# Performance work log

Measured on AMD Instinct MI355X. Metric: run time of the kernel, lower is better.

The kernel has to match this reference:

```python
import jax, jax.numpy as jnp
import numpy as np

B, T, C, H, L, V = 2, 2048, 1024, 16, 6, 32000
D = C // H
FF = 4 * C
EPS = 1e-5


def setup_inputs() -> dict:
    key = jax.random.key(0)
    ks = iter(jax.random.split(key, 32))
    s = 0.02
    inp = {
        "src": jax.random.randint(next(ks), (B, T), 0, V),
        "src_emb": jax.random.normal(next(ks), (V, C), jnp.float32) * s,
        "pos_emb": jax.random.normal(next(ks), (T, C), jnp.float32) * s,
        # stacked per-layer params, leading dim L
        "ln1_w": jnp.ones((L, C), jnp.float32),
        "ln1_b": jnp.zeros((L, C), jnp.float32),
        "wq": jax.random.normal(next(ks), (L, C, C), jnp.float32) * s,
        "bq": jnp.zeros((L, C), jnp.float32),
        "wk": jax.random.normal(next(ks), (L, C, C), jnp.float32) * s,
        "bk": jnp.zeros((L, C), jnp.float32),
        "wv": jax.random.normal(next(ks), (L, C, C), jnp.float32) * s,
        "bv": jnp.zeros((L, C), jnp.float32),
        "wo": jax.random.normal(next(ks), (L, C, C), jnp.float32) * s,
        "bo": jnp.zeros((L, C), jnp.float32),
        "ln2_w": jnp.ones((L, C), jnp.float32),
        "ln2_b": jnp.zeros((L, C), jnp.float32),
        "w1": jax.random.normal(next(ks), (L, C, FF), jnp.float32) * s,
        "b1": jnp.zeros((L, FF), jnp.float32),
        "w2": jax.random.normal(next(ks), (L, FF, C), jnp.float32) * s,
        "b2": jnp.zeros((L, C), jnp.float32),
        "lnf_w": jnp.ones((C,), jnp.float32),
        "lnf_b": jnp.zeros((C,), jnp.float32),
        "head_w": jax.random.normal(next(ks), (C, V), jnp.float32) * s,
    }
    return inp


def _layer_norm(x, w, b):
    mu = jnp.mean(x, axis=-1, keepdims=True)
    var = jnp.mean(jnp.square(x - mu), axis=-1, keepdims=True)
    return (x - mu) * jax.lax.rsqrt(var + EPS) * w + b


def _forward(src, src_emb, pos_emb, layer_params, lnf_w, lnf_b, head_w):
    x = src_emb[src] + pos_emb[jnp.arange(T)][None, :, :]  # [B,T,C]

    def block(x, p):
        (ln1w, ln1b, wq, bq, wk, bk, wv, bv, wo, bo,
         ln2w, ln2b, w1, b1, w2, b2) = p
        h = _layer_norm(x, ln1w, ln1b)
        q = (h @ wq + bq).reshape(B, T, H, D).transpose(0, 2, 1, 3)  # bhtd
        k = (h @ wk + bk).reshape(B, T, H, D).transpose(0, 2, 1, 3)
        v = (h @ wv + bv).reshape(B, T, H, D).transpose(0, 2, 1, 3)
        scores = jnp.einsum('bhtd,bhsd->bhts', q, k) / jnp.sqrt(jnp.float32(D))
        attn = jax.nn.softmax(scores, axis=-1)
        o = jnp.einsum('bhts,bhsd->bhtd', attn, v)
        o = o.transpose(0, 2, 1, 3).reshape(B, T, C)
        x = x + (o @ wo + bo)
        h2 = _layer_norm(x, ln2w, ln2b)
        ff = jax.nn.gelu(h2 @ w1 + b1, approximate=False) @ w2 + b2
        return x + ff, None

    x, _ = jax.lax.scan(block, x, layer_params)
    x = _layer_norm(x, lnf_w, lnf_b)
    return x @ head_w  # [B,T,V] logits


def reference(src, src_emb, pos_emb, ln1_w, ln1_b, wq, bq, wk, bk, wv, bv,
              wo, bo, ln2_w, ln2_b, w1, b1, w2, b2, lnf_w, lnf_b, head_w):
    layer_params = (ln1_w, ln1_b, wq, bq, wk, bk, wv, bv, wo, bo,
                    ln2_w, ln2_b, w1, b1, w2, b2)
    return _forward(src, src_emb, pos_emb, layer_params, lnf_w, lnf_b, head_w)
```

## Files before the change

kernel.cpp:

```cpp
#include <hip/hip_runtime.h>
#include <math.h>

#define BB 2
#define TT 2048
#define CC 1024
#define HH 16
#define LL 6
#define VV 32000
#define DD 64
#define FFF 4096
#define MM (BB*TT)

typedef __bf16 bf16;
typedef __bf16 bf16x8 __attribute__((ext_vector_type(8)));
typedef __bf16 bf16x4 __attribute__((ext_vector_type(4)));
typedef float  floatx4 __attribute__((ext_vector_type(4)));

__device__ __forceinline__ void async_copy16(const void* g, void* l) {
    __builtin_amdgcn_global_load_lds(
        (const __attribute__((address_space(1))) void*)g,
        (__attribute__((address_space(3))) void*)l, 16, 0, 0);
}

template<int BM, int BN, int WM, int WN, int MODE>
__global__ __launch_bounds__(256) void gemm_bt(
    const bf16* __restrict__ A, int lda,
    const bf16* __restrict__ Bt, int ldb,
    int K, void* outp, int ldo,
    const float* __restrict__ bias, const float* res, float scale)
{
    constexpr int MI = WM / 16, NI = WN / 16;
    constexpr int WAVES_N = BN / WN;
    static_assert((BM % 64) == 0 && (BN % 64) == 0, "staging passes");
    static_assert((BM / WM) * (BN / WN) == 4, "4 waves");
    __shared__ __align__(16) bf16 As[BM * 32];
    __shared__ __align__(16) bf16 Bs[BN * 32];

    const int t   = threadIdx.x;
    const int bn0 = blockIdx.x * BN;
    const int bm0 = blockIdx.y * BM;
    const int z   = blockIdx.z;

    if (MODE == 1) {
        size_t ho = (size_t)(z / HH) * TT;
        A  += ho * lda + (z % HH) * DD;
        Bt += ho * ldb + (z % HH) * DD;
    }
    if (MODE == 2) {
        A  += (size_t)z * TT * TT;
        Bt += (size_t)z * DD * TT;
    }

    const int lane = t & 63;
    const int ln   = lane & 15;
    const int quad = lane >> 4;
    const int wave = t >> 6;
    const int wm0  = (wave / WAVES_N) * WM;
    const int wn0  = (wave % WAVES_N) * WN;

    floatx4 acc[MI][NI] = {};

    const int arow = t >> 2;
    const int acol = (t & 3) * 8;

    for (int k0 = 0; k0 < K; k0 += 32) {
#pragma unroll
        for (int p = 0; p < BM / 64; ++p)
            async_copy16(A + (size_t)(bm0 + p * 64 + arow) * lda + k0 + acol,
                         As + p * 2048 + t * 8);
#pragma unroll
        for (int p = 0; p < BN / 64; ++p)
            async_copy16(Bt + (size_t)(bn0 + p * 64 + arow) * ldb + k0 + acol,
                         Bs + p * 2048 + t * 8);
        __syncthreads();
        bf16x8 af[MI], bfv[NI];
#pragma unroll
        for (int i = 0; i < MI; ++i)
            af[i] = *(const bf16x8*)(As + (wm0 + i * 16 + ln) * 32 + quad * 8);
#pragma unroll
        for (int j = 0; j < NI; ++j)
            bfv[j] = *(const bf16x8*)(Bs + (wn0 + j * 16 + ln) * 32 + quad * 8);
#pragma unroll
        for (int i = 0; i < MI; ++i)
#pragma unroll
            for (int j = 0; j < NI; ++j)
                acc[i][j] = __builtin_amdgcn_mfma_f32_16x16x32_bf16(
                    af[i], bfv[j], acc[i][j], 0, 0, 0);
        __syncthreads();
    }

#pragma unroll
    for (int i = 0; i < MI; ++i) {
#pragma unroll
        for (int j = 0; j < NI; ++j) {
            const int n = bn0 + wn0 + j * 16 + ln;
            float bv = 0.0f;
            if (MODE == 0 || MODE == 3 || MODE == 4) bv = bias[n];
#pragma unroll
            for (int r = 0; r < 4; ++r) {
                const int m = bm0 + wm0 + i * 16 + quad * 4 + r;
                float v = acc[i][j][r];
                if (MODE == 1) v *= scale;
                if (MODE == 0 || MODE == 3 || MODE == 4) v += bv;
                if (MODE == 3) v = 0.5f * v * (1.0f + erff(v * 0.70710678118654752f));
                if (MODE == 0 || MODE == 3) {
                    ((bf16*)outp)[(size_t)m * ldo + n] = (bf16)v;
                } else if (MODE == 1) {
                    bf16* o = (bf16*)outp + (size_t)z * TT * TT;
                    o[(size_t)m * TT + n] = (bf16)v;
                } else if (MODE == 2) {
                    bf16* o = (bf16*)outp + (size_t)(z / HH) * TT * CC + (size_t)(z % HH) * DD;
                    o[(size_t)m * CC + n] = (bf16)v;
                } else if (MODE == 4) {
                    float* o = (float*)outp;
                    o[(size_t)m * ldo + n] = v + res[(size_t)m * ldo + n];
                } else {
                    ((float*)outp)[(size_t)m * ldo + n] = v;
                }
            }
        }
    }
}

__global__ void wtrans_kernel(const float* __restrict__ in, bf16* __restrict__ out,
                              int R, int Cc, long long in_bs, long long out_bs)
{
    __shared__ float tile[32][33];
    const float* ip = in  + (size_t)blockIdx.z * in_bs;
    bf16*        op = out + (size_t)blockIdx.z * out_bs;
    int c0 = blockIdx.x * 32, r0 = blockIdx.y * 32;
    int tx = threadIdx.x, ty = threadIdx.y;
#pragma unroll
    for (int r = 0; r < 4; ++r)
        tile[ty + r * 8][tx] = ip[(size_t)(r0 + ty + r * 8) * Cc + c0 + tx];
    __syncthreads();
#pragma unroll
    for (int r = 0; r < 4; ++r)
        op[(size_t)(c0 + ty + r * 8) * R + r0 + tx] = (bf16)tile[tx][ty + r * 8];
}

__global__ void vtrans_kernel(const bf16* __restrict__ qkv, bf16* __restrict__ vT)
{
    __shared__ bf16 tile[32][33];
    int z = blockIdx.z;
    int b = z / HH, h = z % HH;
    int s0 = blockIdx.x * 32, d0 = blockIdx.y * 32;
    int tx = threadIdx.x, ty = threadIdx.y;
    const bf16* in = qkv + (size_t)b * TT * 3 * CC + 2 * CC + h * DD;
#pragma unroll
    for (int r = 0; r < 4; ++r)
        tile[ty + r * 8][tx] = in[(size_t)(s0 + ty + r * 8) * 3 * CC + d0 + tx];
    __syncthreads();
    bf16* o = vT + (size_t)z * DD * TT;
#pragma unroll
    for (int r = 0; r < 4; ++r)
        o[(size_t)(d0 + ty + r * 8) * TT + s0 + tx] = tile[tx][ty + r * 8];
}

__global__ void bias_concat(const float* __restrict__ bq, const float* __restrict__ bk,
                            const float* __restrict__ bv, float* __restrict__ o)
{
    int l = blockIdx.x, c = threadIdx.x;
    o[(size_t)l * 3 * CC + c]          = bq[(size_t)l * CC + c];
    o[(size_t)l * 3 * CC + CC + c]     = bk[(size_t)l * CC + c];
    o[(size_t)l * 3 * CC + 2 * CC + c] = bv[(size_t)l * CC + c];
}

__global__ void embed_kernel(const int* __restrict__ src, const float* __restrict__ semb,
                             const float* __restrict__ pemb, float* __restrict__ x)
{
    int m = blockIdx.x, t = threadIdx.x;
    int tok = src[m];
    int pos = m % TT;
    float4 e = ((const float4*)(semb + (size_t)tok * CC))[t];
    float4 p = ((const float4*)(pemb + (size_t)pos * CC))[t];
    float4 o; o.x = e.x + p.x; o.y = e.y + p.y; o.z = e.z + p.z; o.w = e.w + p.w;
    ((float4*)(x + (size_t)m * CC))[t] = o;
}

__global__ __launch_bounds__(256) void ln_kernel(
    const float* __restrict__ x, const float* __restrict__ w,
    const float* __restrict__ b, bf16* __restrict__ out)
{
    __shared__ float red[4];
    int row = blockIdx.x, t = threadIdx.x;
    float4 v = ((const float4*)(x + (size_t)row * CC))[t];
    float s = v.x + v.y + v.z + v.w;
    for (int off = 32; off; off >>= 1) s += __shfl_xor(s, off, 64);
    if ((t & 63) == 0) red[t >> 6] = s;
    __syncthreads();
    s = red[0] + red[1] + red[2] + red[3];
    float mean = s * (1.0f / CC);
    float dx = v.x - mean, dy = v.y - mean, dz = v.z - mean, dw = v.w - mean;
    float q = dx * dx + dy * dy + dz * dz + dw * dw;
    __syncthreads();
    for (int off = 32; off; off >>= 1) q += __shfl_xor(q, off, 64);
    if ((t & 63) == 0) red[t >> 6] = q;
    __syncthreads();
    q = red[0] + red[1] + red[2] + red[3];
    float rstd = rsqrtf(q * (1.0f / CC) + 1e-5f);
    float4 wv = ((const float4*)w)[t];
    float4 bv = ((const float4*)b)[t];
    bf16x4 ov;
    ov[0] = (bf16)(dx * rstd * wv.x + bv.x);
    ov[1] = (bf16)(dy * rstd * wv.y + bv.y);
    ov[2] = (bf16)(dz * rstd * wv.z + bv.z);
    ov[3] = (bf16)(dw * rstd * wv.w + bv.w);
    *(bf16x4*)(out + (size_t)row * CC + t * 4) = ov;
}

__global__ __launch_bounds__(256) void softmax_kernel(bf16* __restrict__ scores)
{
    __shared__ float red[4];
    bf16* p = scores + (size_t)blockIdx.x * TT;
    int t = threadIdx.x;
    bf16x8 v8 = *(bf16x8*)(p + t * 8);
    float v[8];
    float mx = -1e30f;
#pragma unroll
    for (int i = 0; i < 8; ++i) { v[i] = (float)v8[i]; mx = fmaxf(mx, v[i]); }
    for (int off = 32; off; off >>= 1) mx = fmaxf(mx, __shfl_xor(mx, off, 64));
    if ((t & 63) == 0) red[t >> 6] = mx;
    __syncthreads();
    mx = fmaxf(fmaxf(red[0], red[1]), fmaxf(red[2], red[3]));
    float s = 0.0f;
#pragma unroll
    for (int i = 0; i < 8; ++i) { v[i] = __expf(v[i] - mx); s += v[i]; }
    __syncthreads();
    for (int off = 32; off; off >>= 1) s += __shfl_xor(s, off, 64);
    if ((t & 63) == 0) red[t >> 6] = s;
    __syncthreads();
    s = red[0] + red[1] + red[2] + red[3];
    float inv = 1.0f / s;
#pragma unroll
    for (int i = 0; i < 8; ++i) v8[i] = (bf16)(v[i] * inv);
    *(bf16x8*)(p + t * 8) = v8;
}

extern "C" void kernel_launch(void* const* d_in, const int* in_sizes, int n_in,
                              void* d_out, int out_size, void* d_ws, size_t ws_size,
                              hipStream_t stream)
{
    const int*   src     = (const int*)  d_in[0];
    const float* src_emb = (const float*)d_in[1];
    const float* pos_emb = (const float*)d_in[2];
    const float* ln1_w   = (const float*)d_in[3];
    const float* ln1_b   = (const float*)d_in[4];
    const float* wq      = (const float*)d_in[5];
    const float* bq      = (const float*)d_in[6];
    const float* wk      = (const float*)d_in[7];
    const float* bk      = (const float*)d_in[8];
    const float* wv      = (const float*)d_in[9];
    const float* bv      = (const float*)d_in[10];
    const float* wo      = (const float*)d_in[11];
    const float* bo      = (const float*)d_in[12];
    const float* ln2_w   = (const float*)d_in[13];
    const float* ln2_b   = (const float*)d_in[14];
    const float* w1      = (const float*)d_in[15];
    const float* b1      = (const float*)d_in[16];
    const float* w2      = (const float*)d_in[17];
    const float* b2      = (const float*)d_in[18];
    const float* lnf_w   = (const float*)d_in[19];
    const float* lnf_b   = (const float*)d_in[20];
    const float* head_w  = (const float*)d_in[21];

    char* ob = (char*)d_out;
    bf16* wqkvT  = (bf16*)(ob);
    bf16* woT    = (bf16*)(ob +  37748736);
    bf16* w1T    = (bf16*)(ob +  50331648);
    bf16* w2T    = (bf16*)(ob + 100663296);
    bf16* scores = (bf16*)(ob + 150994944);
    bf16* ff     = (bf16*)(ob + 419430400);
    bf16* qkv    = (bf16*)(ob + 452984832);
    bf16* vT     = (bf16*)(ob + 478150656);
    bf16* obuf   = (bf16*)(ob + 486539264);

    char* wb = (char*)d_ws;
    bf16*  headT = (bf16*)(wb);
    float* x     = (float*)(wb + 65536000);
    bf16*  h     = (bf16*)(wb + 82313216);
    float* bqkv  = (float*)(wb + 90701824);
    if (ws_size < 90775552) return;

    dim3 tb(32, 8, 1);
    long long cc = (long long)CC * CC, cf = (long long)CC * FFF;
    wtrans_kernel<<<dim3(32, 32, LL), tb, 0, stream>>>(wq, wqkvT,              CC, CC, cc, 3 * cc);
    wtrans_kernel<<<dim3(32, 32, LL), tb, 0, stream>>>(wk, wqkvT + CC * CC,    CC, CC, cc, 3 * cc);
    wtrans_kernel<<<dim3(32, 32, LL), tb, 0, stream>>>(wv, wqkvT + 2 * CC * CC, CC, CC, cc, 3 * cc);
    wtrans_kernel<<<dim3(32, 32, LL), tb, 0, stream>>>(wo, woT, CC, CC, cc, cc);
    wtrans_kernel<<<dim3(FFF / 32, CC / 32, LL), tb, 0, stream>>>(w1, w1T, CC, FFF, cf, cf);
    wtrans_kernel<<<dim3(CC / 32, FFF / 32, LL), tb, 0, stream>>>(w2, w2T, FFF, CC, cf, cf);
    wtrans_kernel<<<dim3(VV / 32, CC / 32, 1), tb, 0, stream>>>(head_w, headT, CC, VV, 0, 0);
    bias_concat<<<LL, CC, 0, stream>>>(bq, bk, bv, bqkv);
    embed_kernel<<<MM, 256, 0, stream>>>(src, src_emb, pos_emb, x);

    for (int l = 0; l < LL; ++l) {
        ln_kernel<<<MM, 256, 0, stream>>>(x, ln1_w + l * CC, ln1_b + l * CC, h);
        gemm_bt<128, 128, 64, 64, 0><<<dim3(3 * CC / 128, MM / 128, 1), 256, 0, stream>>>(
            h, CC, wqkvT + (size_t)l * 3 * CC * CC, CC, CC,
            qkv, 3 * CC, bqkv + l * 3 * CC, nullptr, 1.0f);
        vtrans_kernel<<<dim3(TT / 32, DD / 32, BB * HH), tb, 0, stream>>>(qkv, vT);
        gemm_bt<128, 128, 64, 64, 1><<<dim3(TT / 128, TT / 128, BB * HH), 256, 0, stream>>>(
            qkv, 3 * CC, qkv + CC, 3 * CC, DD,
            scores, TT, nullptr, nullptr, 0.125f);
        softmax_kernel<<<BB * HH * TT, 256, 0, stream>>>(scores);
        gemm_bt<128, 64, 32, 64, 2><<<dim3(1, TT / 128, BB * HH), 256, 0, stream>>>(
            scores, TT, vT, TT, TT,
            obuf, CC, nullptr, nullptr, 1.0f);
        gemm_bt<128, 128, 64, 64, 4><<<dim3(CC / 128, MM / 128, 1), 256, 0, stream>>>(
            obuf, CC, woT + (size_t)l * CC * CC, CC, CC,
            x, CC, bo + l * CC, x, 1.0f);
        ln_kernel<<<MM, 256, 0, stream>>>(x, ln2_w + l * CC, ln2_b + l * CC, h);
        gemm_bt<128, 128, 64, 64, 3><<<dim3(FFF / 128, MM / 128, 1), 256, 0, stream>>>(
            h, CC, w1T + (size_t)l * CC * FFF, CC, CC,
            ff, FFF, b1 + l * FFF, nullptr, 1.0f);
        gemm_bt<128, 128, 64, 64, 4><<<dim3(CC / 128, MM / 128, 1), 256, 0, stream>>>(
            ff, FFF, w2T + (size_t)l * CC * FFF, FFF, FFF,
            x, CC, b2 + l * CC, x, 1.0f);
    }
    ln_kernel<<<MM, 256, 0, stream>>>(x, lnf_w, lnf_b, h);
    gemm_bt<128, 128, 64, 64, 5><<<dim3(VV / 128, MM / 128, 1), 256, 0, stream>>>(
        h, CC, headT, CC, CC,
        d_out, VV, nullptr, nullptr, 1.0f);
}
```

Baseline: 4.593 ms.

## Replace materialized attention with fused flash-style attention kernel

Replaces the per-layer score GEMM, separate softmax pass and P·V GEMM with one fused kernel that streams K and V tiles through LDS using swizzled layouts, keeps an online softmax in registers, and writes normalized output directly. This removes the large bf16 score-matrix round trips through global memory. It also adds an XCD-aware grouped block remapping for the final vocabulary-projection GEMM to improve L2 reuse. The fused kernel has only four waves per block and no overlap between loading and computing each tile.

```diff
diff --git a/kernel.cpp b/kernel.cpp
--- a/kernel.cpp
+++ b/kernel.cpp
@@ -37,18 +37,21 @@
     __shared__ __align__(16) bf16 Bs[BN * 32];
 
     const int t   = threadIdx.x;
-    const int bn0 = blockIdx.x * BN;
-    const int bm0 = blockIdx.y * BM;
+    int bn0 = blockIdx.x * BN;
+    int bm0 = blockIdx.y * BM;
     const int z   = blockIdx.z;
 
-    if (MODE == 1) {
-        size_t ho = (size_t)(z / HH) * TT;
-        A  += ho * lda + (z % HH) * DD;
-        Bt += ho * ldb + (z % HH) * DD;
-    }
-    if (MODE == 2) {
-        A  += (size_t)z * TT * TT;
-        Bt += (size_t)z * DD * TT;
+    if (MODE == 5) {
+        const int nwg   = (int)(gridDim.x * gridDim.y);
+        const int flat  = (int)(blockIdx.y * gridDim.x + blockIdx.x);
+        const int chunk = nwg >> 3;
+        const int wg    = (flat & 7) * chunk + (flat >> 3);
+        const int GM    = 8;
+        const int width = GM * (int)gridDim.x;
+        const int g     = wg / width;
+        const int idx   = wg % width;
+        bm0 = (g * GM + (idx % GM)) * BM;
+        bn0 = (idx / GM) * BN;
     }
 
     const int lane = t & 63;
@@ -100,17 +103,10 @@
             for (int r = 0; r < 4; ++r) {
                 const int m = bm0 + wm0 + i * 16 + quad * 4 + r;
                 float v = acc[i][j][r];
-                if (MODE == 1) v *= scale;
                 if (MODE == 0 || MODE == 3 || MODE == 4) v += bv;
                 if (MODE == 3) v = 0.5f * v * (1.0f + erff(v * 0.70710678118654752f));
                 if (MODE == 0 || MODE == 3) {
                     ((bf16*)outp)[(size_t)m * ldo + n] = (bf16)v;
-                } else if (MODE == 1) {
-                    bf16* o = (bf16*)outp + (size_t)z * TT * TT;
-                    o[(size_t)m * TT + n] = (bf16)v;
-                } else if (MODE == 2) {
-                    bf16* o = (bf16*)outp + (size_t)(z / HH) * TT * CC + (size_t)(z % HH) * DD;
-                    o[(size_t)m * CC + n] = (bf16)v;
                 } else if (MODE == 4) {
                     float* o = (float*)outp;
                     o[(size_t)m * ldo + n] = v + res[(size_t)m * ldo + n];
@@ -119,6 +115,125 @@
                 }
             }
         }
+    }
+}
+
+__global__ __launch_bounds__(256) void attn_kernel(
+    const bf16* __restrict__ qkv, const bf16* __restrict__ vT,
+    bf16* __restrict__ obuf)
+{
+    __shared__ __align__(16) bf16 Ks[128 * 64];
+    __shared__ __align__(16) bf16 Vs[64 * 128];
+    __shared__ __align__(16) bf16 Ps[64 * 128];
+
+    const int t    = threadIdx.x;
+    const int lane = t & 63;
+    const int ln   = lane & 15;
+    const int quad = lane >> 4;
+    const int w    = t >> 6;
+    const int q0   = blockIdx.x * 64;
+    const int z    = blockIdx.y;
+    const int b    = z >> 4;
+    const int h    = z & 15;
+
+    const bf16* qp = qkv + (size_t)(b * TT + q0 + w * 16 + ln) * (3 * CC) + h * DD + quad * 8;
+    bf16x8 qf[2];
+#pragma unroll
+    for (int s = 0; s < 2; ++s) {
+        bf16x8 raw = *(const bf16x8*)(qp + s * 32);
+#pragma unroll
+        for (int e = 0; e < 8; ++e) qf[s][e] = (bf16)((float)raw[e] * 0.125f);
+    }
+
+    floatx4 acc_o[4] = {};
+    float m_r[4], l_r[4];
+#pragma unroll
+    for (int r = 0; r < 4; ++r) { m_r[r] = -1e30f; l_r[r] = 0.0f; }
+
+    const int krow = t >> 3;
+    const int kcol = ((t & 7) ^ (krow & 7)) * 8;
+    const bf16* kg = qkv + (size_t)b * TT * (3 * CC) + CC + h * DD + kcol;
+    const int vrow = t >> 4;
+    const int vcol = ((t & 15) ^ (vrow & 15)) * 8;
+    const bf16* vg = vT + (size_t)z * DD * TT + vcol;
+
+    for (int j = 0; j < 16; ++j) {
+#pragma unroll
+        for (int p = 0; p < 4; ++p)
+            async_copy16(kg + (size_t)(j * 128 + p * 32 + krow) * (3 * CC),
+                         Ks + p * 2048 + t * 8);
+#pragma unroll
+        for (int p = 0; p < 4; ++p)
+            async_copy16(vg + (size_t)(p * 16 + vrow) * TT + j * 128,
+                         Vs + p * 2048 + t * 8);
+        __syncthreads();
+
+        floatx4 acc_s[8];
+#pragma unroll
+        for (int nj = 0; nj < 8; ++nj) acc_s[nj] = floatx4{0.f, 0.f, 0.f, 0.f};
+#pragma unroll
+        for (int s = 0; s < 2; ++s) {
+#pragma unroll
+            for (int nj = 0; nj < 8; ++nj) {
+                const int row = nj * 16 + ln;
+                const int cb  = (s * 64 + quad * 16) ^ ((row & 7) << 4);
+                bf16x8 kf = *(const bf16x8*)((const char*)Ks + row * 128 + cb);
+                acc_s[nj] = __builtin_amdgcn_mfma_f32_16x16x32_bf16(qf[s], kf, acc_s[nj], 0, 0, 0);
+            }
+        }
+
+#pragma unroll
+        for (int r = 0; r < 4; ++r) {
+            float v = fmaxf(fmaxf(fmaxf(acc_s[0][r], acc_s[1][r]), fmaxf(acc_s[2][r], acc_s[3][r])),
+                            fmaxf(fmaxf(acc_s[4][r], acc_s[5][r]), fmaxf(acc_s[6][r], acc_s[7][r])));
+            v = fmaxf(v, __shfl_xor(v, 1, 64));
+            v = fmaxf(v, __shfl_xor(v, 2, 64));
+            v = fmaxf(v, __shfl_xor(v, 4, 64));
+            v = fmaxf(v, __shfl_xor(v, 8, 64));
+            const float mn   = fmaxf(m_r[r], v);
+            const float corr = __expf(m_r[r] - mn);
+            m_r[r] = mn;
+#pragma unroll
+            for (int nd = 0; nd < 4; ++nd) acc_o[nd][r] *= corr;
+            const int prow = w * 16 + quad * 4 + r;
+            float rs = 0.0f;
+#pragma unroll
+            for (int nj = 0; nj < 8; ++nj) {
+                float pv = __expf(acc_s[nj][r] - mn);
+                rs += pv;
+                const int cb = (2 * (nj * 16 + ln)) ^ ((prow & 15) << 4);
+                *(bf16*)((char*)Ps + prow * 256 + cb) = (bf16)pv;
+            }
+            rs += __shfl_xor(rs, 1, 64);
+            rs += __shfl_xor(rs, 2, 64);
+            rs += __shfl_xor(rs, 4, 64);
+            rs += __shfl_xor(rs, 8, 64);
+            l_r[r] = l_r[r] * corr + rs;
+        }
+
+#pragma unroll
+        for (int s = 0; s < 4; ++s) {
+            const int prow = w * 16 + ln;
+            const int pcb  = (s * 64 + quad * 16) ^ ((prow & 15) << 4);
+            bf16x8 pa = *(const bf16x8*)((const char*)Ps + prow * 256 + pcb);
+#pragma unroll
+            for (int nd = 0; nd < 4; ++nd) {
+                const int drow = nd * 16 + ln;
+                const int vcb  = (s * 64 + quad * 16) ^ ((drow & 15) << 4);
+                bf16x8 vf = *(const bf16x8*)((const char*)Vs + drow * 256 + vcb);
+                acc_o[nd] = __builtin_amdgcn_mfma_f32_16x16x32_bf16(pa, vf, acc_o[nd], 0, 0, 0);
+            }
+        }
+        __syncthreads();
+    }
+
+    const size_t orow = (size_t)(b * TT + q0 + w * 16 + quad * 4);
+#pragma unroll
+    for (int r = 0; r < 4; ++r) {
+        const float inv = 1.0f / l_r[r];
+#pragma unroll
+        for (int nd = 0; nd < 4; ++nd)
+            obuf[(orow + r) * CC + h * DD + nd * 16 + ln] = (bf16)(acc_o[nd][r] * inv);
     }
 }
 
@@ -209,34 +324,6 @@
     *(bf16x4*)(out + (size_t)row * CC + t * 4) = ov;
 }
 
-__global__ __launch_bounds__(256) void softmax_kernel(bf16* __restrict__ scores)
-{
-    __shared__ float red[4];
-    bf16* p = scores + (size_t)blockIdx.x * TT;
-    int t = threadIdx.x;
-    bf16x8 v8 = *(bf16x8*)(p + t * 8);
-    float v[8];
-    float mx = -1e30f;
-#pragma unroll
-    for (int i = 0; i < 8; ++i) { v[i] = (float)v8[i]; mx = fmaxf(mx, v[i]); }
-    for (int off = 32; off; off >>= 1) mx = fmaxf(mx, __shfl_xor(mx, off, 64));
-    if ((t & 63) == 0) red[t >> 6] = mx;
-    __syncthreads();
-    mx = fmaxf(fmaxf(red[0], red[1]), fmaxf(red[2], red[3]));
-    float s = 0.0f;
-#pragma unroll
-    for (int i = 0; i < 8; ++i) { v[i] = __expf(v[i] - mx); s += v[i]; }
-    __syncthreads();
-    for (int off = 32; off; off >>= 1) s += __shfl_xor(s, off, 64);
-    if ((t & 63) == 0) red[t >> 6] = s;
-    __syncthreads();
-    s = red[0] + red[1] + red[2] + red[3];
-    float inv = 1.0f / s;
-#pragma unroll
-    for (int i = 0; i < 8; ++i) v8[i] = (bf16)(v[i] * inv);
-    *(bf16x8*)(p + t * 8) = v8;
-}
-
 extern "C" void kernel_launch(void* const* d_in, const int* in_sizes, int n_in,
                               void* d_out, int out_size, void* d_ws, size_t ws_size,
                               hipStream_t stream)
@@ -269,7 +356,6 @@
     bf16* woT    = (bf16*)(ob +  37748736);
     bf16* w1T    = (bf16*)(ob +  50331648);
     bf16* w2T    = (bf16*)(ob + 100663296);
-    bf16* scores = (bf16*)(ob + 150994944);
     bf16* ff     = (bf16*)(ob + 419430400);
     bf16* qkv    = (bf16*)(ob + 452984832);
     bf16* vT     = (bf16*)(ob + 478150656);
@@ -300,13 +386,7 @@
             h, CC, wqkvT + (size_t)l * 3 * CC * CC, CC, CC,
             qkv, 3 * CC, bqkv + l * 3 * CC, nullptr, 1.0f);
         vtrans_kernel<<<dim3(TT / 32, DD / 32, BB * HH), tb, 0, stream>>>(qkv, vT);
-        gemm_bt<128, 128, 64, 64, 1><<<dim3(TT / 128, TT / 128, BB * HH), 256, 0, stream>>>(
-            qkv, 3 * CC, qkv + CC, 3 * CC, DD,
-            scores, TT, nullptr, nullptr, 0.125f);
-        softmax_kernel<<<BB * HH * TT, 256, 0, stream>>>(scores);
-        gemm_bt<128, 64, 32, 64, 2><<<dim3(1, TT / 128, BB * HH), 256, 0, stream>>>(
-            scores, TT, vT, TT, TT,
-            obuf, CC, nullptr, nullptr, 1.0f);
+        attn_kernel<<<dim3(TT / 64, BB * HH, 1), 256, 0, stream>>>(qkv, vT, obuf);
         gemm_bt<128, 128, 64, 64, 4><<<dim3(CC / 128, MM / 128, 1), 256, 0, stream>>>(
             obuf, CC, woT + (size_t)l * CC * CC, CC, CC,
             x, CC, bo + l * CC, x, 1.0f);
```

After: 3.746 ms. -18.4%, faster.
